# Optimization experiments

Measured on AMD Instinct MI355X. Metric: run time of the kernel, lower is better.

The kernel has to match this reference:

```python
import jax, jax.numpy as jnp
import numpy as np

BATCH, INPUT_DIM, BOND_DIM, OUTPUT_DIM = 1024, 256, 32, 512


def setup_inputs() -> dict:
    key = jax.random.key(0)
    k_x, k_c, k_p = jax.random.split(key, 3)
    # inputs shifted to [0.5, 1.5] so the length-256 matrix-product chain
    # stays in fp32 dynamic range (pure [0,1] inputs underflow the product).
    x = jax.random.uniform(k_x, (BATCH, INPUT_DIM), dtype=jnp.float32) + 0.5
    # cores scaled so each weighted core has spectral norm ~1 (stable chain)
    cores = jax.random.normal(k_c, (INPUT_DIM, BOND_DIM, BOND_DIM), dtype=jnp.float32) * (0.5 / np.sqrt(BOND_DIM))
    projection = jax.random.normal(k_p, (BOND_DIM, BOND_DIM, OUTPUT_DIM), dtype=jnp.float32) * (1.0 / BOND_DIM)
    bias = jnp.zeros((OUTPUT_DIM,), dtype=jnp.float32)
    return {"x": x, "cores": cores, "projection": projection, "bias": bias}


def reference(x, cores, projection, bias):
    # x: [B, N], cores: [N, D, D], projection: [D, D, O], bias: [O]
    B = x.shape[0]
    D = cores.shape[1]
    # boundary state carrying both bond indices (intended MPS semantics)
    init = jnp.ones((B, D, D), dtype=x.dtype)

    def step(state, inp):
        xi, core = inp                      # xi: [B], core: [D, D]
        w = xi[:, None, None] * core        # weighted core: [B, D, D]
        return jnp.matmul(state, w), None   # chain contraction

    state, _ = jax.lax.scan(step, init, (x.T, cores))  # state: [B, D, D]
    # original: transpose [B,l,r]->[B,r,l], flatten, matmul with flattened projection
    out = jnp.einsum('blr,rlo->bo', state, projection) + bias
    return out
```

## Files before the change

### kernel.cpp

```cpp
#include <hip/hip_runtime.h>


#define NSEG   16
#define SEGLEN 16

__global__ __launch_bounds__(256) void mps_k1(const float* __restrict__ x,
                                              const float* __restrict__ cores,
                                              const float* __restrict__ proj,
                                              float* __restrict__ ws) {
    const int blk = blockIdx.x;
    const int t   = threadIdx.x;

    if (blk < NSEG) {
        __shared__ float Ms[32][33];
        __shared__ float Cs[32][33];
        const float* cbase = cores + (size_t)blk * SEGLEN * 1024;
        const int l  = t >> 3;
        const int r0 = (t & 7) * 4;

        {
            float4 v = *(const float4*)(cbase + l * 32 + r0);
            Ms[l][r0 + 0] = v.x; Ms[l][r0 + 1] = v.y;
            Ms[l][r0 + 2] = v.z; Ms[l][r0 + 3] = v.w;
        }
        __syncthreads();

        for (int i = 1; i < SEGLEN; ++i) {
            float4 c = *(const float4*)(cbase + i * 1024 + l * 32 + r0);
            Cs[l][r0 + 0] = c.x; Cs[l][r0 + 1] = c.y;
            Cs[l][r0 + 2] = c.z; Cs[l][r0 + 3] = c.w;
            __syncthreads();

            float a0 = 0.f, a1 = 0.f, a2 = 0.f, a3 = 0.f;
            #pragma unroll
            for (int k = 0; k < 32; ++k) {
                float m = Ms[l][k];
                a0 = fmaf(m, Cs[k][r0 + 0], a0);
                a1 = fmaf(m, Cs[k][r0 + 1], a1);
                a2 = fmaf(m, Cs[k][r0 + 2], a2);
                a3 = fmaf(m, Cs[k][r0 + 3], a3);
            }
            __syncthreads();
            Ms[l][r0 + 0] = a0; Ms[l][r0 + 1] = a1;
            Ms[l][r0 + 2] = a2; Ms[l][r0 + 3] = a3;
            __syncthreads();
        }

        float4 o4;
        o4.x = Ms[l][r0 + 0]; o4.y = Ms[l][r0 + 1];
        o4.z = Ms[l][r0 + 2]; o4.w = Ms[l][r0 + 3];
        *(float4*)(ws + blk * 1024 + l * 32 + r0) = o4;

    } else if (blk < NSEG + 32) {
        const int base = (blk - NSEG) * 512;
        #pragma unroll
        for (int it = 0; it < 2; ++it) {
            int e = base + it * 256 + t;
            int r = e >> 9;
            int o = e & 511;
            float sum = 0.f;
            #pragma unroll
            for (int l = 0; l < 32; ++l)
                sum += proj[(size_t)(r * 32 + l) * 512 + o];
            ws[16384 + e] = sum;
        }

    } else {
        const int wave = t >> 6;
        const int lane = t & 63;
        const int b    = (blk - (NSEG + 32)) * 4 + wave;
        float4 v = *(const float4*)(x + (size_t)b * 256 + lane * 4);
        float p = v.x * v.y * v.z * v.w;
        #pragma unroll
        for (int off = 32; off >= 1; off >>= 1)
            p *= __shfl_xor(p, off, 64);
        if (lane == 0) ws[32768 + b] = p;
    }
}

__global__ __launch_bounds__(512) void mps_k2(float* __restrict__ ws) {
    __shared__ float u[32];
    __shared__ float un[32];
    const int t = threadIdx.x;

    if (t < 32) {
        float sum = 0.f;
        #pragma unroll
        for (int k = 0; k < 32; ++k) sum += ws[k * 32 + t];
        u[t] = sum;
    }
    __syncthreads();

    for (int sgi = 1; sgi < NSEG; ++sgi) {
        if (t < 32) {
            const float* M = ws + sgi * 1024;
            float sum = 0.f;
            #pragma unroll
            for (int k = 0; k < 32; ++k) sum = fmaf(u[k], M[k * 32 + t], sum);
            un[t] = sum;
        }
        __syncthreads();
        if (t < 32) u[t] = un[t];
        __syncthreads();
    }

    const float* P2 = ws + 16384;
    float sum = 0.f;
    #pragma unroll
    for (int r = 0; r < 32; ++r) sum = fmaf(u[r], P2[r * 512 + t], sum);
    ws[33792 + t] = sum;
}

__global__ __launch_bounds__(256) void mps_k3(const float* __restrict__ ws,
                                              const float* __restrict__ bias,
                                              float* __restrict__ out) {
    const int idx = (blockIdx.x * 256 + threadIdx.x) * 4;
    const int b = idx >> 9;
    const int o = idx & 511;
    const float s  = ws[32768 + b];
    const float4 q4 = *(const float4*)(ws + 33792 + o);
    const float4 bi = *(const float4*)(bias + o);
    float4 r;
    r.x = fmaf(s, q4.x, bi.x);
    r.y = fmaf(s, q4.y, bi.y);
    r.z = fmaf(s, q4.z, bi.z);
    r.w = fmaf(s, q4.w, bi.w);
    *(float4*)(out + idx) = r;
}

extern "C" void kernel_launch(void* const* d_in, const int* in_sizes, int n_in,
                              void* d_out, int out_size, void* d_ws, size_t ws_size,
                              hipStream_t stream) {
    const float* x     = (const float*)d_in[0];
    const float* cores = (const float*)d_in[1];
    const float* proj  = (const float*)d_in[2];
    const float* bias  = (const float*)d_in[3];
    float* out = (float*)d_out;
    float* ws  = (float*)d_ws;

    hipLaunchKernelGGL(mps_k1, dim3(NSEG + 32 + 256), dim3(256), 0, stream,
                       x, cores, proj, ws);
    hipLaunchKernelGGL(mps_k2, dim3(1), dim3(512), 0, stream, ws);
    hipLaunchKernelGGL(mps_k3, dim3(512), dim3(256), 0, stream, ws, bias, out);
}
```

Measured before the change: 88.13 us.

## Fuse chain reduction with output broadcast and preload segment cores into LDS

Three kernels become two. The second kernel now redundantly recomputes the 16-segment vector chain in each of 128 blocks and writes the bias-added output directly, which removes the third launch and the serial single-block step. The first kernel uses 512 threads, preloads a whole 16-core segment into shared memory at once, and ping-pongs two state buffers, cutting per-step global loads and one barrier per step. The cost is redundant chain work in every block and about 64KB of LDS per block, which may limit occupancy.

```diff
diff --git a/kernel.cpp b/kernel.cpp
--- a/kernel.cpp
+++ b/kernel.cpp
@@ -4,7 +4,7 @@
 #define NSEG   16
 #define SEGLEN 16
 
-__global__ __launch_bounds__(256) void mps_k1(const float* __restrict__ x,
+__global__ __launch_bounds__(512) void mps_k1(const float* __restrict__ x,
                                               const float* __restrict__ cores,
                                               const float* __restrict__ proj,
                                               float* __restrict__ ws) {
@@ -12,63 +12,65 @@
     const int t   = threadIdx.x;
 
     if (blk < NSEG) {
-        __shared__ float Ms[32][33];
-        __shared__ float Cs[32][33];
-        const float* cbase = cores + (size_t)blk * SEGLEN * 1024;
-        const int l  = t >> 3;
-        const int r0 = (t & 7) * 4;
-
-        {
-            float4 v = *(const float4*)(cbase + l * 32 + r0);
-            Ms[l][r0 + 0] = v.x; Ms[l][r0 + 1] = v.y;
-            Ms[l][r0 + 2] = v.z; Ms[l][r0 + 3] = v.w;
+        __shared__ float Craw[SEGLEN * 1024];
+        __shared__ float M0[32][33];
+        __shared__ float M1[32][33];
+        const float* cbase = cores + (size_t)blk * (SEGLEN * 1024);
+        #pragma unroll
+        for (int j = 0; j < 8; ++j) {
+            int f = j * 2048 + t * 4;
+            *(float4*)&Craw[f] = *(const float4*)(cbase + f);
         }
+        const int l  = t >> 4;
+        const int c0 = (t & 15) * 2;
         __syncthreads();
 
+        M0[l][c0]     = Craw[l * 32 + c0];
+        M0[l][c0 + 1] = Craw[l * 32 + c0 + 1];
+        __syncthreads();
+
+        float (*pin)[33]  = M0;
+        float (*pout)[33] = M1;
         for (int i = 1; i < SEGLEN; ++i) {
-            float4 c = *(const float4*)(cbase + i * 1024 + l * 32 + r0);
-            Cs[l][r0 + 0] = c.x; Cs[l][r0 + 1] = c.y;
-            Cs[l][r0 + 2] = c.z; Cs[l][r0 + 3] = c.w;
+            const float* Ci = &Craw[i * 1024];
+            float a0 = 0.f, a1 = 0.f, b0 = 0.f, b1 = 0.f;
+            #pragma unroll
+            for (int k = 0; k < 32; k += 2) {
+                float p0 = pin[l][k];
+                float p1 = pin[l][k + 1];
+                float2 c00 = *(const float2*)&Ci[k * 32 + c0];
+                float2 c10 = *(const float2*)&Ci[(k + 1) * 32 + c0];
+                a0 = fmaf(p0, c00.x, a0);
+                a1 = fmaf(p0, c00.y, a1);
+                b0 = fmaf(p1, c10.x, b0);
+                b1 = fmaf(p1, c10.y, b1);
+            }
+            pout[l][c0]     = a0 + b0;
+            pout[l][c0 + 1] = a1 + b1;
             __syncthreads();
-
-            float a0 = 0.f, a1 = 0.f, a2 = 0.f, a3 = 0.f;
-            #pragma unroll
-            for (int k = 0; k < 32; ++k) {
-                float m = Ms[l][k];
-                a0 = fmaf(m, Cs[k][r0 + 0], a0);
-                a1 = fmaf(m, Cs[k][r0 + 1], a1);
-                a2 = fmaf(m, Cs[k][r0 + 2], a2);
-                a3 = fmaf(m, Cs[k][r0 + 3], a3);
-            }
-            __syncthreads();
-            Ms[l][r0 + 0] = a0; Ms[l][r0 + 1] = a1;
-            Ms[l][r0 + 2] = a2; Ms[l][r0 + 3] = a3;
-            __syncthreads();
+            float (*tmp)[33] = pin; pin = pout; pout = tmp;
         }
-
-        float4 o4;
-        o4.x = Ms[l][r0 + 0]; o4.y = Ms[l][r0 + 1];
-        o4.z = Ms[l][r0 + 2]; o4.w = Ms[l][r0 + 3];
-        *(float4*)(ws + blk * 1024 + l * 32 + r0) = o4;
+        *(float2*)(ws + blk * 1024 + l * 32 + c0) =
+            make_float2(pin[l][c0], pin[l][c0 + 1]);
 
     } else if (blk < NSEG + 32) {
-        const int base = (blk - NSEG) * 512;
+        const int e = (blk - NSEG) * 512 + t;
+        const int r = e >> 9;
+        const int o = e & 511;
+        float s0 = 0.f, s1 = 0.f, s2 = 0.f, s3 = 0.f;
         #pragma unroll
-        for (int it = 0; it < 2; ++it) {
-            int e = base + it * 256 + t;
-            int r = e >> 9;
-            int o = e & 511;
-            float sum = 0.f;
-            #pragma unroll
-            for (int l = 0; l < 32; ++l)
-                sum += proj[(size_t)(r * 32 + l) * 512 + o];
-            ws[16384 + e] = sum;
+        for (int l = 0; l < 32; l += 4) {
+            s0 += proj[(size_t)(r * 32 + l) * 512 + o];
+            s1 += proj[(size_t)(r * 32 + l + 1) * 512 + o];
+            s2 += proj[(size_t)(r * 32 + l + 2) * 512 + o];
+            s3 += proj[(size_t)(r * 32 + l + 3) * 512 + o];
         }
+        ws[16384 + e] = (s0 + s1) + (s2 + s3);
 
     } else {
         const int wave = t >> 6;
         const int lane = t & 63;
-        const int b    = (blk - (NSEG + 32)) * 4 + wave;
+        const int b    = (blk - (NSEG + 32)) * 8 + wave;
         float4 v = *(const float4*)(x + (size_t)b * 256 + lane * 4);
         float p = v.x * v.y * v.z * v.w;
         #pragma unroll
@@ -78,54 +80,63 @@
     }
 }
 
-__global__ __launch_bounds__(512) void mps_k2(float* __restrict__ ws) {
+__global__ __launch_bounds__(512) void mps_k2(const float* __restrict__ ws,
+                                              const float* __restrict__ bias,
+                                              float* __restrict__ out) {
+    __shared__ float M[NSEG * 1024];
     __shared__ float u[32];
-    __shared__ float un[32];
     const int t = threadIdx.x;
 
-    if (t < 32) {
-        float sum = 0.f;
-        #pragma unroll
-        for (int k = 0; k < 32; ++k) sum += ws[k * 32 + t];
-        u[t] = sum;
+    #pragma unroll
+    for (int j = 0; j < 8; ++j) {
+        int f = j * 2048 + t * 4;
+        *(float4*)&M[f] = *(const float4*)(ws + f);
     }
     __syncthreads();
 
-    for (int sgi = 1; sgi < NSEG; ++sgi) {
-        if (t < 32) {
-            const float* M = ws + sgi * 1024;
-            float sum = 0.f;
+    if (t < 32) {
+        float s0 = 0.f, s1 = 0.f, s2 = 0.f, s3 = 0.f;
+        #pragma unroll
+        for (int k = 0; k < 32; k += 4) {
+            s0 += M[(k + 0) * 32 + t];
+            s1 += M[(k + 1) * 32 + t];
+            s2 += M[(k + 2) * 32 + t];
+            s3 += M[(k + 3) * 32 + t];
+        }
+        u[t] = (s0 + s1) + (s2 + s3);
+        for (int i = 1; i < NSEG; ++i) {
+            const float* Mi = &M[i * 1024];
+            float a0 = 0.f, a1 = 0.f, a2 = 0.f, a3 = 0.f;
             #pragma unroll
-            for (int k = 0; k < 32; ++k) sum = fmaf(u[k], M[k * 32 + t], sum);
-            un[t] = sum;
+            for (int k = 0; k < 32; k += 4) {
+                a0 = fmaf(u[k + 0], Mi[(k + 0) * 32 + t], a0);
+                a1 = fmaf(u[k + 1], Mi[(k + 1) * 32 + t], a1);
+                a2 = fmaf(u[k + 2], Mi[(k + 2) * 32 + t], a2);
+                a3 = fmaf(u[k + 3], Mi[(k + 3) * 32 + t], a3);
+            }
+            u[t] = (a0 + a1) + (a2 + a3);
         }
-        __syncthreads();
-        if (t < 32) u[t] = un[t];
-        __syncthreads();
     }
+    __syncthreads();
 
     const float* P2 = ws + 16384;
-    float sum = 0.f;
+    float q0 = 0.f, q1 = 0.f, q2 = 0.f, q3 = 0.f;
     #pragma unroll
-    for (int r = 0; r < 32; ++r) sum = fmaf(u[r], P2[r * 512 + t], sum);
-    ws[33792 + t] = sum;
-}
+    for (int r = 0; r < 32; r += 4) {
+        q0 = fmaf(u[r + 0], P2[(r + 0) * 512 + t], q0);
+        q1 = fmaf(u[r + 1], P2[(r + 1) * 512 + t], q1);
+        q2 = fmaf(u[r + 2], P2[(r + 2) * 512 + t], q2);
+        q3 = fmaf(u[r + 3], P2[(r + 3) * 512 + t], q3);
+    }
+    const float qv = (q0 + q1) + (q2 + q3);
+    const float bv = bias[t];
 
-__global__ __launch_bounds__(256) void mps_k3(const float* __restrict__ ws,
-                                              const float* __restrict__ bias,
-                                              float* __restrict__ out) {
-    const int idx = (blockIdx.x * 256 + threadIdx.x) * 4;
-    const int b = idx >> 9;
-    const int o = idx & 511;
-    const float s  = ws[32768 + b];
-    const float4 q4 = *(const float4*)(ws + 33792 + o);
-    const float4 bi = *(const float4*)(bias + o);
-    float4 r;
-    r.x = fmaf(s, q4.x, bi.x);
-    r.y = fmaf(s, q4.y, bi.y);
-    r.z = fmaf(s, q4.z, bi.z);
-    r.w = fmaf(s, q4.w, bi.w);
-    *(float4*)(out + idx) = r;
+    const int b0 = blockIdx.x * 8;
+    #pragma unroll
+    for (int j = 0; j < 8; ++j) {
+        const float s = ws[32768 + b0 + j];
+        out[(size_t)(b0 + j) * 512 + t] = fmaf(s, qv, bv);
+    }
 }
 
 extern "C" void kernel_launch(void* const* d_in, const int* in_sizes, int n_in,
@@ -138,8 +149,7 @@
     float* out = (float*)d_out;
     float* ws  = (float*)d_ws;
 
-    hipLaunchKernelGGL(mps_k1, dim3(NSEG + 32 + 256), dim3(256), 0, stream,
+    hipLaunchKernelGGL(mps_k1, dim3(NSEG + 32 + 128), dim3(512), 0, stream,
                        x, cores, proj, ws);
-    hipLaunchKernelGGL(mps_k2, dim3(1), dim3(512), 0, stream, ws);
-    hipLaunchKernelGGL(mps_k3, dim3(512), dim3(256), 0, stream, ws, bias, out);
+    hipLaunchKernelGGL(mps_k2, dim3(128), dim3(512), 0, stream, ws, bias, out);
 }
```

New measurement: 82.24 us. 1.07x faster.
